# Performance work log

Measured on AMD Instinct MI355X. Metric: run time of the kernel, lower is better.

Reference implementation:

```python
import jax, jax.numpy as jnp
import numpy as np

H = 4  # head_num
K_CONV = 1  # convolution_num


def mhsa_mean(x, Wq, Wk, Wv, Wo):
    # x: [..., L, d]; standard multi-head self-attention followed by mean over L
    d = x.shape[-1]
    hd = d // H
    q = (x @ Wq).reshape(x.shape[:-1] + (H, hd))
    k = (x @ Wk).reshape(x.shape[:-1] + (H, hd))
    v = (x @ Wv).reshape(x.shape[:-1] + (H, hd))
    scores = jnp.einsum('...lhd,...mhd->...hlm', q, k) / jnp.sqrt(jnp.asarray(hd, x.dtype))
    attn = jax.nn.softmax(scores, axis=-1)
    o = jnp.einsum('...hlm,...mhd->...lhd', attn, v).reshape(x.shape) @ Wo
    return o.mean(axis=-2)


def setup_inputs() -> dict:
    key = jax.random.key(0)
    ks = jax.random.split(key, 18)
    WORD, QUERY, ENT, REV = 50000, 50000, 100000, 100000
    DW, DE = 64, 64
    LQ, LR, E, B = 8, 8, 2000000, 1024
    W_word = jax.random.normal(ks[0], (WORD, DW), jnp.float32) * 0.02
    W_word = W_word.at[0].set(0.0)  # padding_idx=0
    W_query = jax.random.normal(ks[1], (QUERY, DE), jnp.float32) * 0.02
    W_entity = jax.random.normal(ks[2], (ENT, DE), jnp.float32) * 0.02
    Wq = jax.random.normal(ks[3], (DW, DW), jnp.float32) * 0.05
    Wk = jax.random.normal(ks[4], (DW, DW), jnp.float32) * 0.05
    Wv = jax.random.normal(ks[5], (DW, DW), jnp.float32) * 0.05
    Wo = jax.random.normal(ks[6], (DW, DW), jnp.float32) * 0.05
    query_word_ids = jax.random.randint(ks[7], (QUERY, LQ), 0, WORD)
    review_word_ids = jax.random.randint(ks[8], (REV, LR), 0, WORD)
    profile_dst = jax.random.randint(ks[9], (REV,), 0, ENT)
    p_src = jax.random.randint(ks[10], (E,), 0, ENT)
    p_dst = jax.random.randint(ks[11], (E,), 0, ENT)
    p_qid = jax.random.randint(ks[12], (E,), 0, QUERY)
    users = jax.random.randint(ks[13], (B,), 0, ENT)
    items = jax.random.randint(ks[14], (B,), 0, ENT)
    negs = jax.random.randint(ks[15], (B,), 0, ENT)
    query_words = jax.random.randint(ks[16], (B, LQ), 0, WORD)
    return {'W_word': W_word, 'W_query': W_query, 'W_entity': W_entity,
            'Wq': Wq, 'Wk': Wk, 'Wv': Wv, 'Wo': Wo,
            'query_word_ids': query_word_ids, 'review_word_ids': review_word_ids,
            'profile_dst': profile_dst, 'p_src': p_src, 'p_dst': p_dst, 'p_qid': p_qid,
            'users': users, 'items': items, 'negs': negs, 'query_words': query_words}


def reference(W_word, W_query, W_entity, Wq, Wk, Wv, Wo,
              query_word_ids, review_word_ids, profile_dst, p_src, p_dst, p_qid,
              users, items, negs, query_words):
    N = W_entity.shape[0]
    DE = W_query.shape[1]
    # --- doc embeddings via MHSA+mean over composing words ---
    h_query = mhsa_mean(W_word[query_word_ids], Wq, Wk, Wv, Wo)    # [Q, DW]
    h_review = mhsa_mean(W_word[review_word_ids], Wq, Wk, Wv, Wo)  # [R, DW]
    # --- profiles: sum reviews into entities, degree-normalize ---
    deg_p = jnp.maximum(jax.ops.segment_sum(jnp.ones(profile_dst.shape[0], jnp.float32), profile_dst, num_segments=N), 1.0)
    ent_h = jax.ops.segment_sum(h_review, profile_dst, num_segments=N) / deg_p[:, None]
    q_e0 = jnp.concatenate([W_query, h_query], axis=-1)   # [Q, D]
    e_k = jnp.concatenate([W_entity, ent_h], axis=-1)     # e_0 [N, D]
    # --- interaction degrees: out-deg(purchased) + out-deg(purchased_by) ---
    ones_e = jnp.ones(p_src.shape[0], jnp.float32)
    deg_i = jax.ops.segment_sum(ones_e, p_src, num_segments=N) + jax.ops.segment_sum(ones_e, p_dst, num_segments=N)
    inv_sqrt = 1.0 / jnp.sqrt(jnp.maximum(deg_i, 1.0))    # [N]
    q_edge = q_e0[p_qid]                                   # [E, D]
    e_acc = e_k
    for _ in range(K_CONV):
        # purchased: m = src.e_k + q_e0[q_id] / sqrt(deg_i[src]); sum to dst
        msg = e_k[p_src] + q_edge * inv_sqrt[p_src][:, None]
        agg = jax.ops.segment_sum(msg, p_dst, num_segments=N)
        # purchased_by (reverse edges): m = e_k[src]/sqrt(deg_i[src]); sum to dst
        agg = agg + jax.ops.segment_sum(e_k[p_dst] * inv_sqrt[p_dst][:, None], p_src, num_segments=N)
        e_k = agg * inv_sqrt[:, None]
        e_acc = e_acc + e_k
    e = e_acc / (K_CONV + 1)                               # [N, D]
    # --- batch forward (train mode) ---
    qb = mhsa_mean(W_word[query_words], Wq, Wk, Wv, Wo)    # [B, DW]
    qb = jnp.concatenate([jnp.zeros((qb.shape[0], DE), qb.dtype), qb], axis=-1)
    personalized = e[users] + qb
    return personalized, e[items], e[negs]
```

## Files before the change

kernel.cpp:

```cpp
#include <hip/hip_runtime.h>

typedef unsigned int uint;
typedef unsigned short ushort;

typedef __bf16 bf16x8 __attribute__((ext_vector_type(8)));
typedef float f32x4 __attribute__((ext_vector_type(4)));
union U8 { uint4 u4; uint w[4]; bf16x8 b; };

__device__ __forceinline__ float bf2f(ushort u) {
    return __uint_as_float(((uint)u) << 16);
}
__device__ __forceinline__ float2 bfp2f(uint u) {
    float2 r;
    r.x = __uint_as_float(u << 16);
    r.y = __uint_as_float(u & 0xffff0000u);
    return r;
}
__device__ __forceinline__ ushort f2bf(float f) {
    uint u = __float_as_uint(f);
    return (ushort)((u + 0x7fffu + ((u >> 16) & 1u)) >> 16);
}
__device__ __forceinline__ uint4 pack8(float4 a, float4 b) {
    uint4 u;
    u.x = (uint)f2bf(a.x) | ((uint)f2bf(a.y) << 16);
    u.y = (uint)f2bf(a.z) | ((uint)f2bf(a.w) << 16);
    u.z = (uint)f2bf(b.x) | ((uint)f2bf(b.y) << 16);
    u.w = (uint)f2bf(b.z) | ((uint)f2bf(b.w) << 16);
    return u;
}

__global__ void mark_kernel(const int* __restrict__ users,
                            const int* __restrict__ items,
                            const int* __restrict__ negs,
                            int* __restrict__ mapid, int* __restrict__ mcnt,
                            int B) {
    int t = blockIdx.x * blockDim.x + threadIdx.x;
    if (t >= 3 * B) return;
    int n = t < B ? users[t] : (t < 2 * B ? items[t - B] : negs[t - 2 * B]);
    int old = atomicCAS(&mapid[n], -1, -2);
    if (old == -1) mapid[n] = atomicAdd(mcnt, 1);
}

__global__ void wswz_kernel(const float* __restrict__ Wq,
                            const float* __restrict__ Wk,
                            const float* __restrict__ Wv,
                            const float* __restrict__ Wo,
                            ushort* __restrict__ wsw, ushort* __restrict__ wswo) {
    int e = blockIdx.x * 256 + threadIdx.x;
    if (e < 12288) {
        int f = e >> 9, r = e & 511;
        int lane = r >> 3, i = r & 7;
        int ct = f >> 1, kh = f & 1;
        int k = kh * 32 + (lane >> 4) * 8 + i;
        int col = (ct & 3) * 16 + (lane & 15);
        const float* W = ct < 4 ? Wq : (ct < 8 ? Wk : Wv);
        wsw[f * 512 + lane * 8 + i] = f2bf(W[k * 64 + col]);
    } else if (e < 16384) {
        int e2 = e - 12288;
        int f = e2 >> 9, r = e2 & 511;
        int lane = r >> 3, i = r & 7;
        int ct = f >> 1, kh = f & 1;
        int k = kh * 32 + (lane >> 4) * 8 + i;
        int col = ct * 16 + (lane & 15);
        wswo[f * 512 + lane * 8 + i] = f2bf(Wo[k * 64 + col]);
    }
}

__global__ void pre_kernel(const float* __restrict__ W_word,
                           const ushort* __restrict__ wsw,
                           ushort* __restrict__ Pq, ushort* __restrict__ Pk,
                           ushort* __restrict__ Pv,
                           const float* __restrict__ W_query,
                           const float* __restrict__ W_entity,
                           ushort* __restrict__ qe0b, ushort* __restrict__ e0b,
                           const int* __restrict__ p_src,
                           const int* __restrict__ p_dst,
                           const int* __restrict__ profile_dst,
                           const int* __restrict__ mapid,
                           int* __restrict__ degp, int* __restrict__ deg2,
                           int WORD, int Qn, int N, int E, int R,
                           int nc_blk, int npj_blk, int ncq_blk, int nce_blk) {
    int bid = blockIdx.x;
    int g = bid >> 3, j = bid & 7;
    if ((g & 3) == 3) {
        int idx = (g >> 2) * 8 + j;
        if (idx >= nc_blk) return;
        int base = idx * 1024 + threadIdx.x;
#pragma unroll
        for (int k = 0; k < 4; k++) {
            int t = base + k * 256;
            if (t < E) {
                int s = p_src[t], d = p_dst[t];
                int md = mapid[d]; if (md >= 0) atomicAdd(&deg2[md], 1);
                int ms = mapid[s]; if (ms >= 0) atomicAdd(&deg2[ms], 1);
            }
            if (t < R) atomicAdd(&degp[profile_dst[t]], 1);
        }
        return;
    }
    int idx = ((g >> 2) * 3 + (g & 3)) * 8 + j;
    if (idx < npj_blk) {
        int tile = idx * 4 + (threadIdx.x >> 6);
        if (tile * 16 >= WORD) return;
        int lane = threadIdx.x & 63, l15 = lane & 15, gi = lane >> 4;
        const float* xr = W_word + ((size_t)tile * 16 + l15) * 64 + gi * 8;
        U8 a0, a1;
        a0.u4 = pack8(*(const float4*)(xr), *(const float4*)(xr + 4));
        a1.u4 = pack8(*(const float4*)(xr + 32), *(const float4*)(xr + 36));
        const f32x4 zero4 = {0.f, 0.f, 0.f, 0.f};
#pragma unroll
        for (int ct = 0; ct < 12; ct++) {
            U8 b0, b1;
            b0.u4 = *(const uint4*)(wsw + (ct * 2 + 0) * 512 + lane * 8);
            b1.u4 = *(const uint4*)(wsw + (ct * 2 + 1) * 512 + lane * 8);
            f32x4 acc = __builtin_amdgcn_mfma_f32_16x16x32_bf16(a0.b, b0.b, zero4, 0, 0, 0);
            acc = __builtin_amdgcn_mfma_f32_16x16x32_bf16(a1.b, b1.b, acc, 0, 0, 0);
            ushort* dst = ct < 4 ? Pq : (ct < 8 ? Pk : Pv);
            int col = (ct & 3) * 16 + l15;
#pragma unroll
            for (int r = 0; r < 4; r++)
                dst[((size_t)tile * 16 + gi * 4 + r) * 64 + col] = f2bf(acc[r]);
        }
    } else if (idx < npj_blk + ncq_blk) {
        int t = (idx - npj_blk) * 256 + threadIdx.x;
        if (t >= Qn * 16) return;
        int r = t >> 4, c = (t & 15) * 4;
        const float4 v = *(const float4*)(W_query + (size_t)r * 64 + c);
        ushort4 o;
        o.x = f2bf(v.x); o.y = f2bf(v.y); o.z = f2bf(v.z); o.w = f2bf(v.w);
        *(ushort4*)(qe0b + (size_t)r * 128 + c) = o;
    } else if (idx < npj_blk + ncq_blk + nce_blk) {
        int t = (idx - npj_blk - ncq_blk) * 256 + threadIdx.x;
        if (t >= N * 16) return;
        int r = t >> 4, c = (t & 15) * 4;
        const float4 v = *(const float4*)(W_entity + (size_t)r * 64 + c);
        ushort4 o;
        o.x = f2bf(v.x); o.y = f2bf(v.y); o.z = f2bf(v.z); o.w = f2bf(v.w);
        *(ushort4*)(e0b + (size_t)r * 128 + c) = o;
    }
}

__global__ void scan_sum(const int* __restrict__ degp, int* __restrict__ csum,
                         int N) {
    __shared__ int red[4];
    int chunk = blockIdx.x, t = threadIdx.x;
    int base = chunk * 1024;
    int v = 0;
#pragma unroll
    for (int k = 0; k < 4; k++) {
        int idx = base + t * 4 + k;
        if (idx < N) v += degp[idx];
    }
#pragma unroll
    for (int o = 32; o; o >>= 1) v += __shfl_down(v, o, 64);
    if ((t & 63) == 0) red[t >> 6] = v;
    __syncthreads();
    if (t == 0) csum[chunk] = red[0] + red[1] + red[2] + red[3];
}

__global__ void scan_mid(int* __restrict__ csum, int nchunk,
                         const int* __restrict__ deg2,
                         int* __restrict__ offs2, int* __restrict__ cursor2,
                         int nb2) {
    __shared__ int lds[256];
    int t = threadIdx.x;
    int v = (t < nchunk) ? csum[t] : 0;
    lds[t] = v;
    __syncthreads();
    for (int o = 1; o < 256; o <<= 1) {
        int u = (t >= o) ? lds[t - o] : 0;
        __syncthreads();
        lds[t] += u;
        __syncthreads();
    }
    if (t < nchunk) csum[t] = lds[t] - v;
    __syncthreads();
    int k2 = nb2 >> 8;
    int s = 0;
    for (int k = 0; k < k2; k++) s += deg2[t * k2 + k];
    lds[t] = s;
    __syncthreads();
    for (int o = 1; o < 256; o <<= 1) {
        int u = (t >= o) ? lds[t - o] : 0;
        __syncthreads();
        lds[t] += u;
        __syncthreads();
    }
    int tb = lds[t] - s;
    for (int k = 0; k < k2; k++) {
        int dv = deg2[t * k2 + k];
        offs2[t * k2 + k] = tb;
        cursor2[t * k2 + k] = tb;
        tb += dv;
    }
    if (t == 255) offs2[nb2] = tb;
}

__global__ void scan_chunk(const int* __restrict__ degp,
                           const int* __restrict__ csum,
                           int* __restrict__ offs_r, int* __restrict__ cursor_r,
                           int N) {
    __shared__ int lds[256];
    int chunk = blockIdx.x, t = threadIdx.x;
    int base = chunk * 1024 + t * 4;
    int v0 = (base + 0 < N) ? degp[base + 0] : 0;
    int v1 = (base + 1 < N) ? degp[base + 1] : 0;
    int v2 = (base + 2 < N) ? degp[base + 2] : 0;
    int v3 = (base + 3 < N) ? degp[base + 3] : 0;
    int s = v0 + v1 + v2 + v3;
    lds[t] = s;
    __syncthreads();
    for (int o = 1; o < 256; o <<= 1) {
        int u = (t >= o) ? lds[t - o] : 0;
        __syncthreads();
        lds[t] += u;
        __syncthreads();
    }
    int tb = lds[t] - s + csum[chunk];
    int vv[4] = {v0, v1, v2, v3};
#pragma unroll
    for (int k = 0; k < 4; k++) {
        int idx = base + k;
        if (idx < N) {
            offs_r[idx] = tb; cursor_r[idx] = tb; tb += vv[k];
            if (idx == N - 1) offs_r[N] = tb;
        }
    }
}

__device__ __forceinline__ void mhsa_pair(const ushort* __restrict__ Pq,
                                          const ushort* __restrict__ Pk,
                                          const ushort* __restrict__ Pv,
                                          const int* __restrict__ ids,
                                          int wid2, int lane,
                                          ushort* __restrict__ outb) {
    const int l15 = lane & 15;
    const int gi  = lane >> 4;
    const int hs  = gi >> 1;
    const int dbase = (gi & 1) * 8;
    const int* idr = ids + (size_t)wid2 * 16;
    const bool valid = hs == (l15 >> 3);

    const int myid = idr[l15];
    int vid[8];
#pragma unroll
    for (int i = 0; i < 8; i++) vid[i] = idr[dbase + i];

    uint pk4[4][2];
    const f32x4 zero4 = {0.f, 0.f, 0.f, 0.f};
#pragma unroll
    for (int h = 0; h < 4; h++) {
        U8 a, b;
        if (valid) {
            a.u4 = *(const uint4*)(Pk + (size_t)myid * 64 + h * 16 + dbase);
            b.u4 = *(const uint4*)(Pq + (size_t)myid * 64 + h * 16 + dbase);
        } else {
            a.u4 = make_uint4(0, 0, 0, 0);
            b.u4 = make_uint4(0, 0, 0, 0);
        }
        f32x4 d = __builtin_amdgcn_mfma_f32_16x16x32_bf16(a.b, b.b, zero4, 0, 0, 0);
        float s0 = d[0] * 0.25f, s1 = d[1] * 0.25f;
        float s2 = d[2] * 0.25f, s3 = d[3] * 0.25f;
        if (!valid) { s0 = s1 = s2 = s3 = -1e30f; }
        float mx = fmaxf(fmaxf(s0, s1), fmaxf(s2, s3));
        mx = fmaxf(mx, __shfl_xor(mx, 16, 64));
        mx = fmaxf(mx, __shfl_xor(mx, 32, 64));
        float x0 = __expf(s0 - mx), x1 = __expf(s1 - mx);
        float x2 = __expf(s2 - mx), x3 = __expf(s3 - mx);
        float sm = x0 + x1 + x2 + x3;
        sm += __shfl_xor(sm, 16, 64);
        sm += __shfl_xor(sm, 32, 64);
        float f = 0.125f / sm;
        uint w0 = (uint)f2bf(x0 * f) | ((uint)f2bf(x1 * f) << 16);
        uint w1 = (uint)f2bf(x2 * f) | ((uint)f2bf(x3 * f) << 16);
        pk4[h][0] = valid ? w0 : 0u;
        pk4[h][1] = valid ? w1 : 0u;
    }

    const int srcA = l15 + (gi & 1) * 32;
    const int srcB = srcA + 16;
    const bool hi = gi >= 2;
    size_t vb[8];
#pragma unroll
    for (int i = 0; i < 8; i++) vb[i] = (size_t)vid[i] * 64;
#pragma unroll
    for (int t = 0; t < 4; t++) {
        uint aw0 = (uint)__shfl((int)pk4[t][0], srcA, 64);
        uint aw1 = (uint)__shfl((int)pk4[t][1], srcA, 64);
        uint aw2 = (uint)__shfl((int)pk4[t][0], srcB, 64);
        uint aw3 = (uint)__shfl((int)pk4[t][1], srcB, 64);
        U8 av_;
        av_.w[0] = hi ? 0u : aw0; av_.w[1] = hi ? 0u : aw1;
        av_.w[2] = hi ? 0u : aw2; av_.w[3] = hi ? 0u : aw3;
        uint e[8];
#pragma unroll
        for (int i = 0; i < 8; i++)
            e[i] = hi ? 0u : (uint)Pv[vb[i] + t * 16 + l15];
        U8 bv;
        bv.w[0] = e[0] | (e[1] << 16);
        bv.w[1] = e[2] | (e[3] << 16);
        bv.w[2] = e[4] | (e[5] << 16);
        bv.w[3] = e[6] | (e[7] << 16);
        f32x4 acc = __builtin_amdgcn_mfma_f32_16x16x32_bf16(av_.b, bv.b, zero4, 0, 0, 0);
        float s = acc[0] + acc[1] + acc[2] + acc[3];
        s += __shfl_xor(s, 16, 64);
        if ((gi & 1) == 0) {
            int row = wid2 * 2 + hs;
            outb[(size_t)row * 64 + t * 16 + l15] = f2bf(s);
        }
    }
}

__global__ void mega_kernel(const ushort* __restrict__ Pq,
                            const ushort* __restrict__ Pk,
                            const ushort* __restrict__ Pv,
                            const int* __restrict__ query_word_ids,
                            const int* __restrict__ review_word_ids,
                            const int* __restrict__ query_words,
                            ushort* __restrict__ hqom,
                            ushort* __restrict__ hrev,
                            ushort* __restrict__ omb,
                            const int* __restrict__ p_src,
                            const int* __restrict__ p_dst,
                            const int* __restrict__ p_qid,
                            const int* __restrict__ profile_dst,
                            const int* __restrict__ mapid,
                            int* __restrict__ degc,
                            int* __restrict__ cursor2, int2* __restrict__ list2,
                            int* __restrict__ cursor_r, int* __restrict__ rmsg,
                            int Qn, int R, int B, int E,
                            int nr_blk, int nq_blk, int nb_blk,
                            int nd_blk, int np_blk, int nv_blk) {
    int bid = blockIdx.x;
    int g = bid >> 3, j = bid & 7;
    int idx = (g >> 1) * 8 + j;
    if (g & 1) {
        if (idx < nd_blk) {
            int base = idx * 1024 + threadIdx.x;
#pragma unroll
            for (int k = 0; k < 4; k++) {
                int t = base + k * 256;
                if (t < E) {
                    atomicAdd(&degc[p_src[t]], 1);
                    atomicAdd(&degc[p_dst[t]], 1);
                }
            }
        } else if (idx < nd_blk + np_blk) {
            int base = (idx - nd_blk) * 512 + threadIdx.x;
#pragma unroll
            for (int k = 0; k < 2; k++) {
                int e = base + k * 256;
                if (e < E) {
                    int s = p_src[e], d = p_dst[e];
                    int md = mapid[d], ms = mapid[s];
                    if (md >= 0)
                        list2[atomicAdd(&cursor2[md], 1)] = make_int2(s, p_qid[e]);
                    if (ms >= 0)
                        list2[atomicAdd(&cursor2[ms], 1)] = make_int2(d, -1);
                }
            }
        } else if (idx < nd_blk + np_blk + nv_blk) {
            int r = (idx - nd_blk - np_blk) * 256 + threadIdx.x;
            if (r >= R) return;
            rmsg[atomicAdd(&cursor_r[profile_dst[r]], 1)] = r;
        }
        return;
    }
    int lane = threadIdx.x & 63;
    int w = threadIdx.x >> 6;
    if (idx < nr_blk) {
        int wid2 = idx * 4 + w;
        if (wid2 < (R >> 1))
            mhsa_pair(Pq, Pk, Pv, review_word_ids, wid2, lane, hrev);
    } else if (idx < nr_blk + nq_blk) {
        int wid2 = (idx - nr_blk) * 4 + w;
        if (wid2 < (Qn >> 1))
            mhsa_pair(Pq, Pk, Pv, query_word_ids, wid2, lane, hqom);
    } else if (idx < nr_blk + nq_blk + nb_blk) {
        int wid2 = (idx - nr_blk - nq_blk) * 4 + w;
        if (wid2 < (B >> 1))
            mhsa_pair(Pq, Pk, Pv, query_words, wid2, lane, omb);
    }
}

__global__ void inv_kernel(const int* __restrict__ degc,
                           float* __restrict__ inv, int N) {
    int t = blockIdx.x * blockDim.x + threadIdx.x;
    if (t >= N) return;
    inv[t] = 1.0f / sqrtf((float)max(degc[t], 1));
}

__global__ void entity_gather(const ushort* __restrict__ hrev,
                              const int* __restrict__ offs_r,
                              const int* __restrict__ rmsg,
                              ushort* __restrict__ eom, int N) {
    int g = (blockIdx.x * blockDim.x + threadIdx.x) >> 4;
    int c = (threadIdx.x & 15) * 4;
    if (g >= N) return;
    int beg = offs_r[g], end = offs_r[g + 1];
    float a0 = 0.f, a1 = 0.f, a2 = 0.f, a3 = 0.f;
    for (int m = beg; m < end; m++) {
        int r = rmsg[m];
        ushort4 v = *(const ushort4*)(hrev + (size_t)r * 64 + c);
        a0 += bf2f(v.x); a1 += bf2f(v.y); a2 += bf2f(v.z); a3 += bf2f(v.w);
    }
    float s = 1.0f / (float)max(end - beg, 1);
    ushort4 o;
    o.x = f2bf(a0 * s); o.y = f2bf(a1 * s); o.z = f2bf(a2 * s); o.w = f2bf(a3 * s);
    *(ushort4*)(eom + (size_t)g * 64 + c) = o;
}

__global__ void wo_kernel(const ushort* __restrict__ eom,
                          const ushort* __restrict__ hqom,
                          const ushort* __restrict__ omb,
                          const ushort* __restrict__ wswo,
                          ushort* __restrict__ e0b, ushort* __restrict__ qe0b,
                          float* __restrict__ qb, int N, int Qn, int B) {
    int tile = blockIdx.x * 4 + (threadIdx.x >> 6);
    int ntile = (N + Qn + B) >> 4;
    if (tile >= ntile) return;
    int lane = threadIdx.x & 63, l15 = lane & 15, gi = lane >> 4;
    int row0 = tile << 4;
    int region; int rb;
    const ushort* src;
    if (row0 < N)            { region = 0; rb = row0;            src = eom; }
    else if (row0 < N + Qn)  { region = 1; rb = row0 - N;        src = hqom; }
    else                     { region = 2; rb = row0 - N - Qn;   src = omb; }
    const ushort* sr = src + ((size_t)rb + l15) * 64;
    U8 a0, a1;
    a0.u4 = *(const uint4*)(sr + gi * 8);
    a1.u4 = *(const uint4*)(sr + 32 + gi * 8);
    const f32x4 zero4 = {0.f, 0.f, 0.f, 0.f};
#pragma unroll
    for (int ct = 0; ct < 4; ct++) {
        U8 b0, b1;
        b0.u4 = *(const uint4*)(wswo + (ct * 2 + 0) * 512 + lane * 8);
        b1.u4 = *(const uint4*)(wswo + (ct * 2 + 1) * 512 + lane * 8);
        f32x4 acc = __builtin_amdgcn_mfma_f32_16x16x32_bf16(a0.b, b0.b, zero4, 0, 0, 0);
        acc = __builtin_amdgcn_mfma_f32_16x16x32_bf16(a1.b, b1.b, acc, 0, 0, 0);
        int col = ct * 16 + l15;
#pragma unroll
        for (int r = 0; r < 4; r++) {
            int row = rb + gi * 4 + r;
            if (region == 0)      e0b[(size_t)row * 128 + 64 + col] = f2bf(acc[r]);
            else if (region == 1) qe0b[(size_t)row * 128 + 64 + col] = f2bf(acc[r]);
            else                  qb[(size_t)row * 64 + col] = acc[r];
        }
    }
}

__global__ void gather_out(const ushort* __restrict__ e0b,
                           const ushort* __restrict__ qe0b,
                           const float* __restrict__ inv,
                           const int* __restrict__ mapid,
                           const int* __restrict__ offs2,
                           const int2* __restrict__ list2,
                           const float* __restrict__ qb,
                           const int* __restrict__ users,
                           const int* __restrict__ items,
                           const int* __restrict__ negs,
                           float* __restrict__ out, int B) {
    int slot = (blockIdx.x * blockDim.x + threadIdx.x) >> 4;
    int c = (threadIdx.x & 15) * 8;
    if (slot >= 3 * B) return;
    int which = slot / B, b = slot - which * B;
    int node = which == 0 ? users[b] : (which == 1 ? items[b] : negs[b]);
    int m = mapid[node];
    int beg = offs2[m], end = offs2[m + 1];
    float a0 = 0.f, a1 = 0.f, a2 = 0.f, a3 = 0.f;
    float a4 = 0.f, a5 = 0.f, a6 = 0.f, a7 = 0.f;
    for (int i = beg; i < end; i++) {
        int2 mm = list2[i];
        float w = inv[mm.x];
        const uint4 ev = *(const uint4*)(e0b + (size_t)mm.x * 128 + c);
        if (mm.y >= 0) {
            const uint4 qv = *(const uint4*)(qe0b + (size_t)mm.y * 128 + c);
            float2 e, q;
            e = bfp2f(ev.x); q = bfp2f(qv.x); a0 += fmaf(q.x, w, e.x); a1 += fmaf(q.y, w, e.y);
            e = bfp2f(ev.y); q = bfp2f(qv.y); a2 += fmaf(q.x, w, e.x); a3 += fmaf(q.y, w, e.y);
            e = bfp2f(ev.z); q = bfp2f(qv.z); a4 += fmaf(q.x, w, e.x); a5 += fmaf(q.y, w, e.y);
            e = bfp2f(ev.w); q = bfp2f(qv.w); a6 += fmaf(q.x, w, e.x); a7 += fmaf(q.y, w, e.y);
        } else {
            float2 e;
            e = bfp2f(ev.x); a0 = fmaf(e.x, w, a0); a1 = fmaf(e.y, w, a1);
            e = bfp2f(ev.y); a2 = fmaf(e.x, w, a2); a3 = fmaf(e.y, w, a3);
            e = bfp2f(ev.z); a4 = fmaf(e.x, w, a4); a5 = fmaf(e.y, w, a5);
            e = bfp2f(ev.w); a6 = fmaf(e.x, w, a6); a7 = fmaf(e.y, w, a7);
        }
    }
    float wn = inv[node];
    const uint4 sv = *(const uint4*)(e0b + (size_t)node * 128 + c);
    float2 e0v;
    float r0, r1, r2, r3, r4, r5, r6, r7;
    e0v = bfp2f(sv.x); r0 = 0.5f * fmaf(a0, wn, e0v.x); r1 = 0.5f * fmaf(a1, wn, e0v.y);
    e0v = bfp2f(sv.y); r2 = 0.5f * fmaf(a2, wn, e0v.x); r3 = 0.5f * fmaf(a3, wn, e0v.y);
    e0v = bfp2f(sv.z); r4 = 0.5f * fmaf(a4, wn, e0v.x); r5 = 0.5f * fmaf(a5, wn, e0v.y);
    e0v = bfp2f(sv.w); r6 = 0.5f * fmaf(a6, wn, e0v.x); r7 = 0.5f * fmaf(a7, wn, e0v.y);
    if (which == 0 && c >= 64) {
        const float4 q0 = *(const float4*)(qb + (size_t)b * 64 + (c - 64));
        const float4 q1 = *(const float4*)(qb + (size_t)b * 64 + (c - 60));
        r0 += q0.x; r1 += q0.y; r2 += q0.z; r3 += q0.w;
        r4 += q1.x; r5 += q1.y; r6 += q1.z; r7 += q1.w;
    }
    float* dst = out + (size_t)which * B * 128 + (size_t)b * 128 + c;
    float4 w0; w0.x = r0; w0.y = r1; w0.z = r2; w0.w = r3;
    float4 w1; w1.x = r4; w1.y = r5; w1.z = r6; w1.w = r7;
    *(float4*)dst = w0;
    *(float4*)(dst + 4) = w1;
}

extern "C" void kernel_launch(void* const* d_in, const int* in_sizes, int n_in,
                              void* d_out, int out_size, void* d_ws, size_t ws_size,
                              hipStream_t stream) {
    const float* W_word   = (const float*)d_in[0];
    const float* W_query  = (const float*)d_in[1];
    const float* W_entity = (const float*)d_in[2];
    const float* Wq       = (const float*)d_in[3];
    const float* Wk       = (const float*)d_in[4];
    const float* Wv       = (const float*)d_in[5];
    const float* Wo       = (const float*)d_in[6];
    const int* query_word_ids  = (const int*)d_in[7];
    const int* review_word_ids = (const int*)d_in[8];
    const int* profile_dst     = (const int*)d_in[9];
    const int* p_src  = (const int*)d_in[10];
    const int* p_dst  = (const int*)d_in[11];
    const int* p_qid  = (const int*)d_in[12];
    const int* users  = (const int*)d_in[13];
    const int* items  = (const int*)d_in[14];
    const int* negs   = (const int*)d_in[15];
    const int* query_words = (const int*)d_in[16];

    const int WORD = in_sizes[0] / 64;
    const int Qn   = in_sizes[1] / 64;
    const int N    = in_sizes[2] / 64;
    const int R    = in_sizes[8] / 8;
    const int E    = in_sizes[10];
    const int B    = in_sizes[13];

    const int NB2 = ((3 * B + 255) / 256) * 256;

    ushort* e0b  = (ushort*)d_ws;
    ushort* qe0b = e0b + (size_t)N * 128;
    ushort* Pq   = qe0b + (size_t)Qn * 128;
    ushort* Pk   = Pq + (size_t)WORD * 64;
    ushort* Pv   = Pk + (size_t)WORD * 64;
    ushort* hrev = Pv + (size_t)WORD * 64;
    ushort* hqom = hrev + (size_t)R * 64;
    ushort* omb  = hqom + (size_t)Qn * 64;
    ushort* eom  = omb + (size_t)B * 64;
    ushort* wsw  = eom + (size_t)N * 64;
    ushort* wswo = wsw + 12288;
    float*  qb   = (float*)(wswo + 4096);
    float*  inv  = qb + (size_t)B * 64;
    int* degc     = (int*)(inv + N);
    int* degp     = degc + N;
    int* deg2     = degp + N;
    int* mcnt     = deg2 + NB2;
    int* mapid    = mcnt + 4;
    int* offs_r   = mapid + N;
    int* cursor_r = offs_r + N + 2;
    int* csum     = cursor_r + N;
    int* offs2    = csum + 256;
    int* cursor2  = offs2 + NB2 + 2;
    int* rmsg     = cursor2 + NB2;
    int2* list2   = (int2*)(rmsg + R);

    const int nchunk = (N + 1023) / 1024;

    hipMemsetAsync(degc, 0, (2 * (size_t)N + NB2 + 4) * sizeof(int), stream);
    hipMemsetAsync(mapid, 0xFF, (size_t)N * sizeof(int), stream);

    mark_kernel<<<(3 * B + 255) / 256, 256, 0, stream>>>(users, items, negs,
                                                         mapid, mcnt, B);
    wswz_kernel<<<64, 256, 0, stream>>>(Wq, Wk, Wv, Wo, wsw, wswo);

    {
        int nc_blk  = (E + 1023) / 1024;
        int npj_blk = (WORD / 16 + 3) / 4;
        int ncq_blk = (Qn * 16 + 255) / 256;
        int nce_blk = (N * 16 + 255) / 256;
        int mh_fam  = npj_blk + ncq_blk + nce_blk;
        int T = max(4 * nc_blk, (mh_fam * 4 + 2) / 3);
        T = ((T + 31) / 32) * 32;
        pre_kernel<<<T, 256, 0, stream>>>(W_word, wsw, Pq, Pk, Pv,
                                          W_query, W_entity, qe0b, e0b,
                                          p_src, p_dst, profile_dst, mapid,
                                          degp, deg2,
                                          WORD, Qn, N, E, R,
                                          nc_blk, npj_blk, ncq_blk, nce_blk);
    }

    scan_sum<<<nchunk, 256, 0, stream>>>(degp, csum, N);
    scan_mid<<<1, 256, 0, stream>>>(csum, nchunk, deg2, offs2, cursor2, NB2);
    scan_chunk<<<nchunk, 256, 0, stream>>>(degp, csum, offs_r, cursor_r, N);

    {
        int nr_blk = (R / 2 + 3) / 4;
        int nq_blk = (Qn / 2 + 3) / 4;
        int nb_blk = (B / 2 + 3) / 4;
        int nd_blk = (E + 1023) / 1024;
        int np_blk = (E + 511) / 512;
        int nv_blk = (R + 255) / 256;
        int sc = nd_blk + np_blk + nv_blk;
        int mh = nr_blk + nq_blk + nb_blk;
        int T = 2 * max(sc, mh);
        T = ((T + 31) / 32) * 32;
        mega_kernel<<<T, 256, 0, stream>>>(Pq, Pk, Pv,
                                           query_word_ids, review_word_ids, query_words,
                                           hqom, hrev, omb,
                                           p_src, p_dst, p_qid, profile_dst, mapid,
                                           degc, cursor2, list2, cursor_r, rmsg,
                                           Qn, R, B, E,
                                           nr_blk, nq_blk, nb_blk,
                                           nd_blk, np_blk, nv_blk);
    }

    inv_kernel<<<(N + 255) / 256, 256, 0, stream>>>(degc, inv, N);

    entity_gather<<<(N * 16 + 255) / 256, 256, 0, stream>>>(hrev, offs_r, rmsg, eom, N);

    {
        int ntile = (N + Qn + B) / 16;
        wo_kernel<<<(ntile + 3) / 4, 256, 0, stream>>>(eom, hqom, omb, wswo,
                                                       e0b, qe0b, qb, N, Qn, B);
    }

    gather_out<<<(3 * B * 16 + 255) / 256, 256, 0, stream>>>(e0b, qe0b, inv,
                                                             mapid, offs2, list2,
                                                             qb, users, items, negs,
                                                             (float*)d_out, B);
}
```

Before: 504.0 us.

## Merge small launches and stripe degree atomics across eight copies

```diff
diff --git a/kernel.cpp b/kernel.cpp
--- a/kernel.cpp
+++ b/kernel.cpp
@@ -29,41 +29,43 @@
     return u;
 }
 
-__global__ void mark_kernel(const int* __restrict__ users,
-                            const int* __restrict__ items,
-                            const int* __restrict__ negs,
-                            int* __restrict__ mapid, int* __restrict__ mcnt,
-                            int B) {
-    int t = blockIdx.x * blockDim.x + threadIdx.x;
+__global__ void setup_kernel(const float* __restrict__ Wq,
+                             const float* __restrict__ Wk,
+                             const float* __restrict__ Wv,
+                             const float* __restrict__ Wo,
+                             ushort* __restrict__ wsw, ushort* __restrict__ wswo,
+                             const int* __restrict__ users,
+                             const int* __restrict__ items,
+                             const int* __restrict__ negs,
+                             int* __restrict__ mapid, int* __restrict__ mcnt,
+                             int B) {
+    int bid = blockIdx.x;
+    if (bid < 64) {
+        int e = bid * 256 + threadIdx.x;
+        if (e < 12288) {
+            int f = e >> 9, r = e & 511;
+            int lane = r >> 3, i = r & 7;
+            int ct = f >> 1, kh = f & 1;
+            int k = kh * 32 + (lane >> 4) * 8 + i;
+            int col = (ct & 3) * 16 + (lane & 15);
+            const float* W = ct < 4 ? Wq : (ct < 8 ? Wk : Wv);
+            wsw[f * 512 + lane * 8 + i] = f2bf(W[k * 64 + col]);
+        } else if (e < 16384) {
+            int e2 = e - 12288;
+            int f = e2 >> 9, r = e2 & 511;
+            int lane = r >> 3, i = r & 7;
+            int ct = f >> 1, kh = f & 1;
+            int k = kh * 32 + (lane >> 4) * 8 + i;
+            int col = ct * 16 + (lane & 15);
+            wswo[f * 512 + lane * 8 + i] = f2bf(Wo[k * 64 + col]);
+        }
+        return;
+    }
+    int t = (bid - 64) * 256 + threadIdx.x;
     if (t >= 3 * B) return;
     int n = t < B ? users[t] : (t < 2 * B ? items[t - B] : negs[t - 2 * B]);
     int old = atomicCAS(&mapid[n], -1, -2);
     if (old == -1) mapid[n] = atomicAdd(mcnt, 1);
-}
-
-__global__ void wswz_kernel(const float* __restrict__ Wq,
-                            const float* __restrict__ Wk,
-                            const float* __restrict__ Wv,
-                            const float* __restrict__ Wo,
-                            ushort* __restrict__ wsw, ushort* __restrict__ wswo) {
-    int e = blockIdx.x * 256 + threadIdx.x;
-    if (e < 12288) {
-        int f = e >> 9, r = e & 511;
-        int lane = r >> 3, i = r & 7;
-        int ct = f >> 1, kh = f & 1;
-        int k = kh * 32 + (lane >> 4) * 8 + i;
-        int col = (ct & 3) * 16 + (lane & 15);
-        const float* W = ct < 4 ? Wq : (ct < 8 ? Wk : Wv);
-        wsw[f * 512 + lane * 8 + i] = f2bf(W[k * 64 + col]);
-    } else if (e < 16384) {
-        int e2 = e - 12288;
-        int f = e2 >> 9, r = e2 & 511;
-        int lane = r >> 3, i = r & 7;
-        int ct = f >> 1, kh = f & 1;
-        int k = kh * 32 + (lane >> 4) * 8 + i;
-        int col = ct * 16 + (lane & 15);
-        wswo[f * 512 + lane * 8 + i] = f2bf(Wo[k * 64 + col]);
-    }
 }
 
 __global__ void pre_kernel(const float* __restrict__ W_word,
@@ -325,10 +327,10 @@
                             const int* __restrict__ p_qid,
                             const int* __restrict__ profile_dst,
                             const int* __restrict__ mapid,
-                            int* __restrict__ degc,
+                            int* __restrict__ degc8,
                             int* __restrict__ cursor2, int2* __restrict__ list2,
                             int* __restrict__ cursor_r, int* __restrict__ rmsg,
-                            int Qn, int R, int B, int E,
+                            int Qn, int R, int B, int E, int N,
                             int nr_blk, int nq_blk, int nb_blk,
                             int nd_blk, int np_blk, int nv_blk) {
     int bid = blockIdx.x;
@@ -336,6 +338,7 @@
     int idx = (g >> 1) * 8 + j;
     if (g & 1) {
         if (idx < nd_blk) {
+            int* degc = degc8 + (size_t)(bid & 7) * N;
             int base = idx * 1024 + threadIdx.x;
 #pragma unroll
             for (int k = 0; k < 4; k++) {
@@ -383,43 +386,16 @@
     }
 }
 
-__global__ void inv_kernel(const int* __restrict__ degc,
-                           float* __restrict__ inv, int N) {
-    int t = blockIdx.x * blockDim.x + threadIdx.x;
-    if (t >= N) return;
-    inv[t] = 1.0f / sqrtf((float)max(degc[t], 1));
-}
-
-__global__ void entity_gather(const ushort* __restrict__ hrev,
-                              const int* __restrict__ offs_r,
-                              const int* __restrict__ rmsg,
-                              ushort* __restrict__ eom, int N) {
-    int g = (blockIdx.x * blockDim.x + threadIdx.x) >> 4;
-    int c = (threadIdx.x & 15) * 4;
-    if (g >= N) return;
-    int beg = offs_r[g], end = offs_r[g + 1];
-    float a0 = 0.f, a1 = 0.f, a2 = 0.f, a3 = 0.f;
-    for (int m = beg; m < end; m++) {
-        int r = rmsg[m];
-        ushort4 v = *(const ushort4*)(hrev + (size_t)r * 64 + c);
-        a0 += bf2f(v.x); a1 += bf2f(v.y); a2 += bf2f(v.z); a3 += bf2f(v.w);
-    }
-    float s = 1.0f / (float)max(end - beg, 1);
-    ushort4 o;
-    o.x = f2bf(a0 * s); o.y = f2bf(a1 * s); o.z = f2bf(a2 * s); o.w = f2bf(a3 * s);
-    *(ushort4*)(eom + (size_t)g * 64 + c) = o;
-}
-
-__global__ void wo_kernel(const ushort* __restrict__ eom,
-                          const ushort* __restrict__ hqom,
-                          const ushort* __restrict__ omb,
-                          const ushort* __restrict__ wswo,
-                          ushort* __restrict__ e0b, ushort* __restrict__ qe0b,
-                          float* __restrict__ qb, int N, int Qn, int B) {
-    int tile = blockIdx.x * 4 + (threadIdx.x >> 6);
-    int ntile = (N + Qn + B) >> 4;
-    if (tile >= ntile) return;
-    int lane = threadIdx.x & 63, l15 = lane & 15, gi = lane >> 4;
+__device__ __forceinline__ void wo_tile(int tile,
+                                        const ushort* __restrict__ eom,
+                                        const ushort* __restrict__ hqom,
+                                        const ushort* __restrict__ omb,
+                                        const ushort* __restrict__ wswo,
+                                        ushort* __restrict__ e0b,
+                                        ushort* __restrict__ qe0b,
+                                        float* __restrict__ qb,
+                                        int N, int Qn, int lane) {
+    int l15 = lane & 15, gi = lane >> 4;
     int row0 = tile << 4;
     int region; int rb;
     const ushort* src;
@@ -447,6 +423,62 @@
             else                  qb[(size_t)row * 64 + col] = acc[r];
         }
     }
+}
+
+__global__ void post1_kernel(const ushort* __restrict__ hrev,
+                             const int* __restrict__ offs_r,
+                             const int* __restrict__ rmsg,
+                             ushort* __restrict__ eom,
+                             const ushort* __restrict__ hqom,
+                             const ushort* __restrict__ omb,
+                             const ushort* __restrict__ wswo,
+                             ushort* __restrict__ e0b, ushort* __restrict__ qe0b,
+                             float* __restrict__ qb,
+                             const int* __restrict__ degc8,
+                             float* __restrict__ inv,
+                             int N, int Qn, int B,
+                             int nent_blk, int nwo_blk) {
+    int bid = blockIdx.x;
+    if (bid < nent_blk) {
+        int g = (bid * 256 + (int)threadIdx.x) >> 4;
+        int c = (threadIdx.x & 15) * 4;
+        if (g >= N) return;
+        int beg = offs_r[g], end = offs_r[g + 1];
+        float a0 = 0.f, a1 = 0.f, a2 = 0.f, a3 = 0.f;
+        for (int m = beg; m < end; m++) {
+            int r = rmsg[m];
+            ushort4 v = *(const ushort4*)(hrev + (size_t)r * 64 + c);
+            a0 += bf2f(v.x); a1 += bf2f(v.y); a2 += bf2f(v.z); a3 += bf2f(v.w);
+        }
+        float s = 1.0f / (float)max(end - beg, 1);
+        ushort4 o;
+        o.x = f2bf(a0 * s); o.y = f2bf(a1 * s); o.z = f2bf(a2 * s); o.w = f2bf(a3 * s);
+        *(ushort4*)(eom + (size_t)g * 64 + c) = o;
+    } else if (bid < nent_blk + nwo_blk) {
+        int ntile = (N + Qn + B) >> 4;
+        int tile = (N >> 4) + (bid - nent_blk) * 4 + ((int)threadIdx.x >> 6);
+        if (tile >= ntile) return;
+        wo_tile(tile, eom, hqom, omb, wswo, e0b, qe0b, qb, N, Qn,
+                threadIdx.x & 63);
+    } else {
+        int t = (bid - nent_blk - nwo_blk) * 256 + threadIdx.x;
+        if (t >= N) return;
+        int s = 0;
+#pragma unroll
+        for (int c = 0; c < 8; c++) s += degc8[(size_t)c * N + t];
+        inv[t] = 1.0f / sqrtf((float)max(s, 1));
+    }
+}
+
+__global__ void post2_kernel(const ushort* __restrict__ eom,
+                             const ushort* __restrict__ hqom,
+                             const ushort* __restrict__ omb,
+                             const ushort* __restrict__ wswo,
+                             ushort* __restrict__ e0b, ushort* __restrict__ qe0b,
+                             float* __restrict__ qb, int N, int Qn, int B) {
+    int tile = blockIdx.x * 4 + ((int)threadIdx.x >> 6);
+    if (tile >= (N >> 4)) return;
+    wo_tile(tile, eom, hqom, omb, wswo, e0b, qe0b, qb, N, Qn, threadIdx.x & 63);
 }
 
 __global__ void gather_out(const ushort* __restrict__ e0b,
@@ -552,8 +584,8 @@
     ushort* wswo = wsw + 12288;
     float*  qb   = (float*)(wswo + 4096);
     float*  inv  = qb + (size_t)B * 64;
-    int* degc     = (int*)(inv + N);
-    int* degp     = degc + N;
+    int* degc8    = (int*)(inv + N);
+    int* degp     = degc8 + 8 * (size_t)N;
     int* deg2     = degp + N;
     int* mcnt     = deg2 + NB2;
     int* mapid    = mcnt + 4;
@@ -567,12 +599,11 @@
 
     const int nchunk = (N + 1023) / 1024;
 
-    hipMemsetAsync(degc, 0, (2 * (size_t)N + NB2 + 4) * sizeof(int), stream);
+    hipMemsetAsync(degc8, 0, (9 * (size_t)N + NB2 + 4) * sizeof(int), stream);
     hipMemsetAsync(mapid, 0xFF, (size_t)N * sizeof(int), stream);
 
-    mark_kernel<<<(3 * B + 255) / 256, 256, 0, stream>>>(users, items, negs,
-                                                         mapid, mcnt, B);
-    wswz_kernel<<<64, 256, 0, stream>>>(Wq, Wk, Wv, Wo, wsw, wswo);
+    setup_kernel<<<64 + (3 * B + 255) / 256, 256, 0, stream>>>(
+        Wq, Wk, Wv, Wo, wsw, wswo, users, items, negs, mapid, mcnt, B);
 
     {
         int nc_blk  = (E + 1023) / 1024;
@@ -609,21 +640,24 @@
                                            query_word_ids, review_word_ids, query_words,
                                            hqom, hrev, omb,
                                            p_src, p_dst, p_qid, profile_dst, mapid,
-                                           degc, cursor2, list2, cursor_r, rmsg,
-                                           Qn, R, B, E,
+                                           degc8, cursor2, list2, cursor_r, rmsg,
+                                           Qn, R, B, E, N,
                                            nr_blk, nq_blk, nb_blk,
                                            nd_blk, np_blk, nv_blk);
     }
 
-    inv_kernel<<<(N + 255) / 256, 256, 0, stream>>>(degc, inv, N);
-
-    entity_gather<<<(N * 16 + 255) / 256, 256, 0, stream>>>(hrev, offs_r, rmsg, eom, N);
-
     {
-        int ntile = (N + Qn + B) / 16;
-        wo_kernel<<<(ntile + 3) / 4, 256, 0, stream>>>(eom, hqom, omb, wswo,
+        int nent_blk = (N * 16 + 255) / 256;
+        int ntile12 = (Qn + B) / 16 + 1;
+        int nwo_blk = (ntile12 + 3) / 4;
+        int ninv_blk = (N + 255) / 256;
+        post1_kernel<<<nent_blk + nwo_blk + ninv_blk, 256, 0, stream>>>(
+            hrev, offs_r, rmsg, eom, hqom, omb, wswo, e0b, qe0b, qb,
+            degc8, inv, N, Qn, B, nent_blk, nwo_blk);
+    }
+
+    post2_kernel<<<(N / 16 + 3) / 4, 256, 0, stream>>>(eom, hqom, omb, wswo,
                                                        e0b, qe0b, qb, N, Qn, B);
-    }
 
     gather_out<<<(3 * B * 16 + 255) / 256, 256, 0, stream>>>(e0b, qe0b, inv,
                                                              mapid, offs2, list2,
```

Result: faster. 488.3 us (median of 2 runs) (-3.1%).
